# Optimization experiments

Measured on AMD Instinct MI355X. Metric: run time of the kernel, lower is better.

## Reference

```python
import jax, jax.numpy as jnp
import numpy as np


def setup_inputs() -> dict:
    key = jax.random.key(0)
    ks = jax.random.split(key, 7)
    B, N, D, A = 32, 128, 512, 512
    sD = 1.0 / np.sqrt(D)
    sA = 1.0 / np.sqrt(A)
    return {
        "x": jax.random.normal(ks[0], (B, N, D), dtype=jnp.float32),
        "W1": jax.random.normal(ks[1], (A, D), dtype=jnp.float32) * sD,
        "b1": jax.random.normal(ks[2], (A,), dtype=jnp.float32) * sD,
        "W2": jax.random.normal(ks[3], (A, D), dtype=jnp.float32) * sD,
        "b2": jax.random.normal(ks[4], (A,), dtype=jnp.float32) * sD,
        "Wout": jax.random.normal(ks[5], (A,), dtype=jnp.float32) * sA,
        "bout": jax.random.normal(ks[6], (1,), dtype=jnp.float32) * sA,
    }


def reference(x, W1, b1, W2, b2, Wout, bout):
    # x: (B, N, D)
    x1 = jnp.einsum('bnd,ad->bna', x, W1) + b1  # mlp1 -> (B, N, A)
    x2 = jnp.einsum('bnd,ad->bna', x, W2) + b2  # mlp2 -> (B, N, A)
    # outer broadcast add: x1.unsqueeze(1) + x2.unsqueeze(2) -> (B, N, N, A)
    s = x1[:, None, :, :] + x2[:, :, None, :]
    # include_root=False: drop ROOT row along dim 1 -> (B, N-1, N, A)
    s = s[:, 1:, :, :]
    s = jnp.tanh(s)
    # out linear A -> 1, then squeeze -> (B, N-1, N)
    return jnp.einsum('bija,a->bij', s, Wout) + bout[0]
```

## Files before the change

kernel.cpp:

```cpp
#include <hip/hip_runtime.h>
#include <hip/hip_bf16.h>

#define B_ 32
#define N_ 128
#define D_ 512
#define A_ 512
#define R_ (B_*N_)
#define OC 1024
#define CEXP 2.8853900817779268f

typedef __attribute__((ext_vector_type(8)))  short frag_ab;
typedef __attribute__((ext_vector_type(16))) float frag_c;

__device__ inline unsigned pack2bf(float a, float b) {
    unsigned ua = __builtin_bit_cast(unsigned, a) + 0x8000u;
    unsigned ub = __builtin_bit_cast(unsigned, b) + 0x8000u;
    return __builtin_amdgcn_perm(ub, ua, 0x07060302);
}
__device__ inline float bf2f_lo(unsigned u){ return __builtin_bit_cast(float, u << 16); }
__device__ inline float bf2f_hi(unsigned u){ return __builtin_bit_cast(float, u & 0xffff0000u); }

__global__ __launch_bounds__(256) void k0_cvt(
    const float* __restrict__ X, const float* __restrict__ W1,
    const float* __restrict__ W2,
    unsigned short* __restrict__ Xb, unsigned short* __restrict__ W1b,
    unsigned short* __restrict__ W2b)
{
    const int NX = R_*D_/8, NW = A_*D_/8;
    int i = blockIdx.x*256 + threadIdx.x;
    const float* src; unsigned short* dst; int off;
    if (i < NX)            { src = X;  dst = Xb;  off = i; }
    else if (i < NX+NW)    { src = W1; dst = W1b; off = i-NX; }
    else if (i < NX+2*NW)  { src = W2; dst = W2b; off = i-NX-NW; }
    else return;
    float4 a = ((const float4*)src)[off*2];
    float4 c = ((const float4*)src)[off*2+1];
    uint4 o;
    o.x = pack2bf(a.x,a.y); o.y = pack2bf(a.z,a.w);
    o.z = pack2bf(c.x,c.y); o.w = pack2bf(c.z,c.w);
    ((uint4*)dst)[off] = o;
}

__global__ __launch_bounds__(256) void k1_mfma(
    const unsigned short* __restrict__ Xb,
    const unsigned short* __restrict__ W1b, const float* __restrict__ b1,
    const unsigned short* __restrict__ W2b, const float* __restrict__ b2,
    unsigned short* __restrict__ Yb)
{
    __shared__ unsigned short As[2][64*64];
    __shared__ unsigned short Bs[2][64*64];

    const int t = threadIdx.x, lane = t&63, wid = t>>6;
    const int wr = wid>>1, wc = wid&1;
    const int row0 = blockIdx.x*64, col0 = blockIdx.y*64;
    const unsigned short* Wb = (col0 < A_) ? W1b : W2b;
    const float* bb = (col0 < A_) ? b1 : b2;
    const int wrow0 = col0 & (A_-1);

    const int sr = t>>2;
    const int ss = (t&3)*2;
    const int sf = sr & 7;

    frag_c acc;
#pragma unroll
    for (int r=0;r<16;++r) acc[r] = 0.f;

    const int fr = lane & 31;
    const int hs = lane >> 5;
    const int arow = wr*32 + fr, af_f = arow & 7;
    const int brow = wc*32 + fr, bf_f = brow & 7;

    {
        const unsigned short* px = &Xb[(size_t)(row0 +sr)*D_ + ss*8];
        const unsigned short* pw = &Wb[(size_t)(wrow0+sr)*D_ + ss*8];
        uint4 a0 = *(const uint4*)px, a1 = *(const uint4*)(px+8);
        uint4 b0 = *(const uint4*)pw, b1v = *(const uint4*)(pw+8);
        *(uint4*)&As[0][sr*64 + (( ss   ^sf)<<3)] = a0;
        *(uint4*)&As[0][sr*64 + (((ss+1)^sf)<<3)] = a1;
        *(uint4*)&Bs[0][sr*64 + (( ss   ^sf)<<3)] = b0;
        *(uint4*)&Bs[0][sr*64 + (((ss+1)^sf)<<3)] = b1v;
    }
    __syncthreads();

#pragma unroll
    for (int s = 0; s < 8; ++s) {
        const int cur = s & 1;
        uint4 a0, a1, b0, b1v;
        if (s < 7) {
            const int k0 = (s+1)*64;
            const unsigned short* px = &Xb[(size_t)(row0 +sr)*D_ + k0 + ss*8];
            const unsigned short* pw = &Wb[(size_t)(wrow0+sr)*D_ + k0 + ss*8];
            a0 = *(const uint4*)px; a1 = *(const uint4*)(px+8);
            b0 = *(const uint4*)pw; b1v = *(const uint4*)(pw+8);
        }
        frag_ab af[4], bf[4];
#pragma unroll
        for (int ks=0; ks<4; ++ks) {
            const int slot = ks*2 + hs;
            af[ks] = *(const frag_ab*)&As[cur][arow*64 + ((slot^af_f)<<3)];
            bf[ks] = *(const frag_ab*)&Bs[cur][brow*64 + ((slot^bf_f)<<3)];
        }
#pragma unroll
        for (int ks=0; ks<4; ++ks)
            acc = __builtin_amdgcn_mfma_f32_32x32x16_bf16(af[ks], bf[ks], acc, 0, 0, 0);
        if (s < 7) {
            *(uint4*)&As[cur^1][sr*64 + (( ss   ^sf)<<3)] = a0;
            *(uint4*)&As[cur^1][sr*64 + (((ss+1)^sf)<<3)] = a1;
            *(uint4*)&Bs[cur^1][sr*64 + (( ss   ^sf)<<3)] = b0;
            *(uint4*)&Bs[cur^1][sr*64 + (((ss+1)^sf)<<3)] = b1v;
        }
        __syncthreads();
    }

    const int cc = col0 + wc*32 + (lane&31);
    const float bias = bb[cc & (A_-1)];
    const int rbase = row0 + wr*32 + 4*(lane>>5);
#pragma unroll
    for (int r=0; r<16; ++r) {
        const int rr = rbase + (r&3) + 8*(r>>2);
        float e = __builtin_amdgcn_exp2f(CEXP*(acc[r] + bias));
        Yb[(size_t)rr*OC + cc] =
            (unsigned short)((__builtin_bit_cast(unsigned, e) + 0x8000u) >> 16);
    }
}

__global__ __launch_bounds__(256) void k2_tanh(
    const unsigned short* __restrict__ Yb,
    const float* __restrict__ Wout,
    float* __restrict__ P)
{
    __shared__ unsigned short e1s[64*64];
    __shared__ unsigned short e2s[64*64];
    __shared__ float wo[64];
    __shared__ float wsum_s;

    const int t  = threadIdx.x;
    const int jt = blockIdx.x & 1;
    const int it = blockIdx.x >> 1;
    const int ac = blockIdx.y;
    const int b  = blockIdx.z;
    const int abase = ac*64;

    if (t < 64) {
        float w = Wout[abase + t];
        wo[t] = w;
#pragma unroll
        for (int off=32; off>=1; off>>=1) w += __shfl_down(w, off, 64);
        if (t == 0) wsum_s = w;
    }

    const unsigned short* yb = Yb + (size_t)b*N_*OC;
    {
        const int r  = t>>2;
        const int s0 = (t&3)*2;
        const int f  = (r>>2)&7;
        int g2 = it*64 + r + 1; if (g2 > 127) g2 = 127;
        const unsigned short* p1 = &yb[(size_t)(jt*64 + r)*OC + abase + s0*8];
        const unsigned short* p2 = &yb[(size_t)g2*OC + A_ + abase + s0*8];
        uint4 a0 = *(const uint4*)p1, a1 = *(const uint4*)(p1+8);
        uint4 b0 = *(const uint4*)p2, b1v = *(const uint4*)(p2+8);
        *(uint4*)&e1s[r*64 + (( s0   ^f)<<3)] = a0;
        *(uint4*)&e1s[r*64 + (((s0+1)^f)<<3)] = a1;
        *(uint4*)&e2s[r*64 + (( s0   ^f)<<3)] = b0;
        *(uint4*)&e2s[r*64 + (((s0+1)^f)<<3)] = b1v;
    }
    __syncthreads();

    const int jl = t&15, il = t>>4;
    const int fj = jl&7, fi = il&7;
    float acc[4][4];
#pragma unroll
    for (int kj=0;kj<4;++kj)
#pragma unroll
        for (int ki=0;ki<4;++ki) acc[kj][ki] = 0.f;

#pragma unroll
    for (int c8=0; c8<8; ++c8) {
        uint4 V4[4];
#pragma unroll
        for (int ki=0;ki<4;++ki)
            V4[ki] = *(const uint4*)&e2s[(4*il+ki)*64 + ((c8^fi)<<3)];
        float vf[4][8];
#pragma unroll
        for (int ki=0;ki<4;++ki) {
            vf[ki][0]=bf2f_lo(V4[ki].x); vf[ki][1]=bf2f_hi(V4[ki].x);
            vf[ki][2]=bf2f_lo(V4[ki].y); vf[ki][3]=bf2f_hi(V4[ki].y);
            vf[ki][4]=bf2f_lo(V4[ki].z); vf[ki][5]=bf2f_hi(V4[ki].z);
            vf[ki][6]=bf2f_lo(V4[ki].w); vf[ki][7]=bf2f_hi(V4[ki].w);
        }
        float4 wa = *(const float4*)&wo[c8*8];
        float4 wb = *(const float4*)&wo[c8*8 + 4];
#pragma unroll
        for (int kj=0;kj<4;++kj) {
            uint4 U = *(const uint4*)&e1s[(4*jl+kj)*64 + ((c8^fj)<<3)];
            float u0=bf2f_lo(U.x), u1=bf2f_hi(U.x), u2=bf2f_lo(U.y), u3=bf2f_hi(U.y);
            float u4=bf2f_lo(U.z), u5=bf2f_hi(U.z), u6=bf2f_lo(U.w), u7=bf2f_hi(U.w);
#pragma unroll
            for (int ki=0;ki<4;++ki) {
                { float r0=fmaf(u0,vf[ki][0],1.f), s0=fmaf(u1,vf[ki][1],1.f);
                  acc[kj][ki]=fmaf(fmaf(wa.x,s0,wa.y*r0),__builtin_amdgcn_rcpf(r0*s0),acc[kj][ki]); }
                { float r0=fmaf(u2,vf[ki][2],1.f), s0=fmaf(u3,vf[ki][3],1.f);
                  acc[kj][ki]=fmaf(fmaf(wa.z,s0,wa.w*r0),__builtin_amdgcn_rcpf(r0*s0),acc[kj][ki]); }
                { float r0=fmaf(u4,vf[ki][4],1.f), s0=fmaf(u5,vf[ki][5],1.f);
                  acc[kj][ki]=fmaf(fmaf(wb.x,s0,wb.y*r0),__builtin_amdgcn_rcpf(r0*s0),acc[kj][ki]); }
                { float r0=fmaf(u6,vf[ki][6],1.f), s0=fmaf(u7,vf[ki][7],1.f);
                  acc[kj][ki]=fmaf(fmaf(wb.z,s0,wb.w*r0),__builtin_amdgcn_rcpf(r0*s0),acc[kj][ki]); }
            }
        }
    }

    const float base = wsum_s;
    float* Pb = P + ((size_t)(ac*B_ + b))*128*128;
#pragma unroll
    for (int ki=0;ki<4;++ki) {
        const int i0 = it*64 + 4*il + ki;
        float4 o = { base - 2.f*acc[0][ki], base - 2.f*acc[1][ki],
                     base - 2.f*acc[2][ki], base - 2.f*acc[3][ki] };
        *(float4*)&Pb[i0*128 + jt*64 + 4*jl] = o;
    }
}

__global__ __launch_bounds__(256) void k3_reduce(
    const float* __restrict__ P, const float* __restrict__ bout,
    float* __restrict__ out)
{
    int o = blockIdx.x*256 + threadIdx.x;
    if (o >= B_*127*128) return;
    const int b = o / (127*128);
    const int rem = o - b*127*128;
    const float* p = P + (size_t)b*16384 + rem;
    float s = bout[0];
#pragma unroll
    for (int q=0; q<8; ++q) s += p[(size_t)q*B_*16384];
    out[o] = s;
}

extern "C" void kernel_launch(void* const* d_in, const int* in_sizes, int n_in,
                              void* d_out, int out_size, void* d_ws, size_t ws_size,
                              hipStream_t stream) {
    const float* x    = (const float*)d_in[0];
    const float* W1   = (const float*)d_in[1];
    const float* b1   = (const float*)d_in[2];
    const float* W2   = (const float*)d_in[3];
    const float* b2   = (const float*)d_in[4];
    const float* Wout = (const float*)d_in[5];
    const float* bout = (const float*)d_in[6];
    float* out = (float*)d_out;

    char* ws = (char*)d_ws;
    unsigned short* Yb  = (unsigned short*)ws;
    unsigned short* Xb  = (unsigned short*)(ws + (8u<<20));
    unsigned short* W1b = (unsigned short*)(ws + (12u<<20));
    unsigned short* W2b = (unsigned short*)(ws + (12u<<20) + (1u<<19));
    float*          P   = (float*)(ws + (16u<<20));

    k0_cvt<<<1280, 256, 0, stream>>>(x, W1, W2, Xb, W1b, W2b);

    dim3 g1(R_/64, OC/64);
    k1_mfma<<<g1, 256, 0, stream>>>(Xb, W1b, b1, W2b, b2, Yb);

    dim3 g2(4, 8, B_);
    k2_tanh<<<g2, 256, 0, stream>>>(Yb, Wout, P);

    k3_reduce<<<(B_*127*128 + 255)/256, 256, 0, stream>>>(P, bout, out);
}
```

Baseline: 122.9 us.

## Fuse bf16 conversion into GEMM and full-A reduction into tanh kernel

The separate fp32-to-bf16 conversion kernel is dropped, and the GEMM now loads fp32 X/W and packs to bf16 while staging into LDS. The pairwise tanh kernel now handles the whole 512-wide A dimension per block, using 32x32 tiles with a 2x2 micro-tile per thread. It writes final outputs with bout directly, which removes the partial-sum buffer P and the k3 reduction launch. The cost is twice the global load bytes in the GEMM, lower ILP per thread in k2, and fewer blocks (512 versus 1024).

Result: slower. 125.9 us (+2.4%).

```diff
diff --git a/kernel.cpp b/kernel.cpp
--- a/kernel.cpp
+++ b/kernel.cpp
@@ -20,31 +20,10 @@
 __device__ inline float bf2f_lo(unsigned u){ return __builtin_bit_cast(float, u << 16); }
 __device__ inline float bf2f_hi(unsigned u){ return __builtin_bit_cast(float, u & 0xffff0000u); }
 
-__global__ __launch_bounds__(256) void k0_cvt(
-    const float* __restrict__ X, const float* __restrict__ W1,
-    const float* __restrict__ W2,
-    unsigned short* __restrict__ Xb, unsigned short* __restrict__ W1b,
-    unsigned short* __restrict__ W2b)
-{
-    const int NX = R_*D_/8, NW = A_*D_/8;
-    int i = blockIdx.x*256 + threadIdx.x;
-    const float* src; unsigned short* dst; int off;
-    if (i < NX)            { src = X;  dst = Xb;  off = i; }
-    else if (i < NX+NW)    { src = W1; dst = W1b; off = i-NX; }
-    else if (i < NX+2*NW)  { src = W2; dst = W2b; off = i-NX-NW; }
-    else return;
-    float4 a = ((const float4*)src)[off*2];
-    float4 c = ((const float4*)src)[off*2+1];
-    uint4 o;
-    o.x = pack2bf(a.x,a.y); o.y = pack2bf(a.z,a.w);
-    o.z = pack2bf(c.x,c.y); o.w = pack2bf(c.z,c.w);
-    ((uint4*)dst)[off] = o;
-}
-
 __global__ __launch_bounds__(256) void k1_mfma(
-    const unsigned short* __restrict__ Xb,
-    const unsigned short* __restrict__ W1b, const float* __restrict__ b1,
-    const unsigned short* __restrict__ W2b, const float* __restrict__ b2,
+    const float* __restrict__ X,
+    const float* __restrict__ W1, const float* __restrict__ b1,
+    const float* __restrict__ W2, const float* __restrict__ b2,
     unsigned short* __restrict__ Yb)
 {
     __shared__ unsigned short As[2][64*64];
@@ -53,7 +32,7 @@
     const int t = threadIdx.x, lane = t&63, wid = t>>6;
     const int wr = wid>>1, wc = wid&1;
     const int row0 = blockIdx.x*64, col0 = blockIdx.y*64;
-    const unsigned short* Wb = (col0 < A_) ? W1b : W2b;
+    const float* Wb = (col0 < A_) ? W1 : W2;
     const float* bb = (col0 < A_) ? b1 : b2;
     const int wrow0 = col0 & (A_-1);
 
@@ -70,28 +49,35 @@
     const int arow = wr*32 + fr, af_f = arow & 7;
     const int brow = wc*32 + fr, bf_f = brow & 7;
 
+    const float* pxb = &X [(size_t)(row0 +sr)*D_ + ss*8];
+    const float* pwb = &Wb[(size_t)(wrow0+sr)*D_ + ss*8];
+
     {
-        const unsigned short* px = &Xb[(size_t)(row0 +sr)*D_ + ss*8];
-        const unsigned short* pw = &Wb[(size_t)(wrow0+sr)*D_ + ss*8];
-        uint4 a0 = *(const uint4*)px, a1 = *(const uint4*)(px+8);
-        uint4 b0 = *(const uint4*)pw, b1v = *(const uint4*)(pw+8);
-        *(uint4*)&As[0][sr*64 + (( ss   ^sf)<<3)] = a0;
-        *(uint4*)&As[0][sr*64 + (((ss+1)^sf)<<3)] = a1;
-        *(uint4*)&Bs[0][sr*64 + (( ss   ^sf)<<3)] = b0;
-        *(uint4*)&Bs[0][sr*64 + (((ss+1)^sf)<<3)] = b1v;
+        float4 x0 = *(const float4*)pxb,     x1 = *(const float4*)(pxb+4);
+        float4 x2 = *(const float4*)(pxb+8), x3 = *(const float4*)(pxb+12);
+        float4 w0 = *(const float4*)pwb,     w1 = *(const float4*)(pwb+4);
+        float4 w2 = *(const float4*)(pwb+8), w3 = *(const float4*)(pwb+12);
+        uint4 A0 = {pack2bf(x0.x,x0.y), pack2bf(x0.z,x0.w), pack2bf(x1.x,x1.y), pack2bf(x1.z,x1.w)};
+        uint4 A1 = {pack2bf(x2.x,x2.y), pack2bf(x2.z,x2.w), pack2bf(x3.x,x3.y), pack2bf(x3.z,x3.w)};
+        uint4 B0 = {pack2bf(w0.x,w0.y), pack2bf(w0.z,w0.w), pack2bf(w1.x,w1.y), pack2bf(w1.z,w1.w)};
+        uint4 B1 = {pack2bf(w2.x,w2.y), pack2bf(w2.z,w2.w), pack2bf(w3.x,w3.y), pack2bf(w3.z,w3.w)};
+        *(uint4*)&As[0][sr*64 + (( ss   ^sf)<<3)] = A0;
+        *(uint4*)&As[0][sr*64 + (((ss+1)^sf)<<3)] = A1;
+        *(uint4*)&Bs[0][sr*64 + (( ss   ^sf)<<3)] = B0;
+        *(uint4*)&Bs[0][sr*64 + (((ss+1)^sf)<<3)] = B1;
     }
     __syncthreads();
 
 #pragma unroll
     for (int s = 0; s < 8; ++s) {
         const int cur = s & 1;
-        uint4 a0, a1, b0, b1v;
+        float4 x0,x1,x2,x3,w0,w1,w2,w3;
         if (s < 7) {
             const int k0 = (s+1)*64;
-            const unsigned short* px = &Xb[(size_t)(row0 +sr)*D_ + k0 + ss*8];
-            const unsigned short* pw = &Wb[(size_t)(wrow0+sr)*D_ + k0 + ss*8];
-            a0 = *(const uint4*)px; a1 = *(const uint4*)(px+8);
-            b0 = *(const uint4*)pw; b1v = *(const uint4*)(pw+8);
+            x0 = *(const float4*)(pxb+k0);    x1 = *(const float4*)(pxb+k0+4);
+            x2 = *(const float4*)(pxb+k0+8);  x3 = *(const float4*)(pxb+k0+12);
+            w0 = *(const float4*)(pwb+k0);    w1 = *(const float4*)(pwb+k0+4);
+            w2 = *(const float4*)(pwb+k0+8);  w3 = *(const float4*)(pwb+k0+12);
         }
         frag_ab af[4], bf[4];
 #pragma unroll
@@ -104,10 +90,14 @@
         for (int ks=0; ks<4; ++ks)
             acc = __builtin_amdgcn_mfma_f32_32x32x16_bf16(af[ks], bf[ks], acc, 0, 0, 0);
         if (s < 7) {
-            *(uint4*)&As[cur^1][sr*64 + (( ss   ^sf)<<3)] = a0;
-            *(uint4*)&As[cur^1][sr*64 + (((ss+1)^sf)<<3)] = a1;
-            *(uint4*)&Bs[cur^1][sr*64 + (( ss   ^sf)<<3)] = b0;
-            *(uint4*)&Bs[cur^1][sr*64 + (((ss+1)^sf)<<3)] = b1v;
+            uint4 A0 = {pack2bf(x0.x,x0.y), pack2bf(x0.z,x0.w), pack2bf(x1.x,x1.y), pack2bf(x1.z,x1.w)};
+            uint4 A1 = {pack2bf(x2.x,x2.y), pack2bf(x2.z,x2.w), pack2bf(x3.x,x3.y), pack2bf(x3.z,x3.w)};
+            uint4 B0 = {pack2bf(w0.x,w0.y), pack2bf(w0.z,w0.w), pack2bf(w1.x,w1.y), pack2bf(w1.z,w1.w)};
+            uint4 B1 = {pack2bf(w2.x,w2.y), pack2bf(w2.z,w2.w), pack2bf(w3.x,w3.y), pack2bf(w3.z,w3.w)};
+            *(uint4*)&As[cur^1][sr*64 + (( ss   ^sf)<<3)] = A0;
+            *(uint4*)&As[cur^1][sr*64 + (((ss+1)^sf)<<3)] = A1;
+            *(uint4*)&Bs[cur^1][sr*64 + (( ss   ^sf)<<3)] = B0;
+            *(uint4*)&Bs[cur^1][sr*64 + (((ss+1)^sf)<<3)] = B1;
         }
         __syncthreads();
     }
@@ -126,113 +116,95 @@
 
 __global__ __launch_bounds__(256) void k2_tanh(
     const unsigned short* __restrict__ Yb,
-    const float* __restrict__ Wout,
-    float* __restrict__ P)
+    const float* __restrict__ Wout, const float* __restrict__ bout,
+    float* __restrict__ out)
 {
-    __shared__ unsigned short e1s[64*64];
-    __shared__ unsigned short e2s[64*64];
-    __shared__ float wo[64];
-    __shared__ float wsum_s;
+    __shared__ unsigned short e1s[32*512];
+    __shared__ unsigned short e2s[32*512];
+    __shared__ float wo[A_];
+    __shared__ float wsum_s[4];
 
     const int t  = threadIdx.x;
-    const int jt = blockIdx.x & 1;
-    const int it = blockIdx.x >> 1;
-    const int ac = blockIdx.y;
-    const int b  = blockIdx.z;
-    const int abase = ac*64;
-
-    if (t < 64) {
-        float w = Wout[abase + t];
-        wo[t] = w;
-#pragma unroll
-        for (int off=32; off>=1; off>>=1) w += __shfl_down(w, off, 64);
-        if (t == 0) wsum_s = w;
+    const int jt = blockIdx.x & 3;
+    const int it = blockIdx.x >> 2;
+    const int b  = blockIdx.y;
+
+    {
+        float w0 = Wout[t], w1 = Wout[256+t];
+        wo[t] = w0; wo[256+t] = w1;
+        float s = w0 + w1;
+#pragma unroll
+        for (int off=32; off>=1; off>>=1) s += __shfl_down(s, off, 64);
+        if ((t&63)==0) wsum_s[t>>6] = s;
     }
 
     const unsigned short* yb = Yb + (size_t)b*N_*OC;
     {
-        const int r  = t>>2;
-        const int s0 = (t&3)*2;
-        const int f  = (r>>2)&7;
-        int g2 = it*64 + r + 1; if (g2 > 127) g2 = 127;
-        const unsigned short* p1 = &yb[(size_t)(jt*64 + r)*OC + abase + s0*8];
-        const unsigned short* p2 = &yb[(size_t)g2*OC + A_ + abase + s0*8];
-        uint4 a0 = *(const uint4*)p1, a1 = *(const uint4*)(p1+8);
-        uint4 b0 = *(const uint4*)p2, b1v = *(const uint4*)(p2+8);
-        *(uint4*)&e1s[r*64 + (( s0   ^f)<<3)] = a0;
-        *(uint4*)&e1s[r*64 + (((s0+1)^f)<<3)] = a1;
-        *(uint4*)&e2s[r*64 + (( s0   ^f)<<3)] = b0;
-        *(uint4*)&e2s[r*64 + (((s0+1)^f)<<3)] = b1v;
+        const int r = t>>3, inner = t&7;
+        const int key = r >> 1;
+        const int g2 = min(it*32 + r + 1, 127);
+        const unsigned short* p1 = &yb[(size_t)(jt*32 + r)*OC + inner*8];
+        const unsigned short* p2 = &yb[(size_t)g2*OC + A_ + inner*8];
+        unsigned short* d1 = &e1s[r*512];
+        unsigned short* d2 = &e2s[r*512];
+#pragma unroll
+        for (int q=0; q<8; ++q) {
+            const int slot = q*8 + inner;
+            uint4 v1 = *(const uint4*)(p1 + q*64);
+            uint4 v2 = *(const uint4*)(p2 + q*64);
+            *(uint4*)&d1[(slot^key)<<3] = v1;
+            *(uint4*)&d2[(slot^key)<<3] = v2;
+        }
     }
     __syncthreads();
 
     const int jl = t&15, il = t>>4;
-    const int fj = jl&7, fi = il&7;
-    float acc[4][4];
-#pragma unroll
-    for (int kj=0;kj<4;++kj)
-#pragma unroll
-        for (int ki=0;ki<4;++ki) acc[kj][ki] = 0.f;
-
-#pragma unroll
-    for (int c8=0; c8<8; ++c8) {
-        uint4 V4[4];
-#pragma unroll
-        for (int ki=0;ki<4;++ki)
-            V4[ki] = *(const uint4*)&e2s[(4*il+ki)*64 + ((c8^fi)<<3)];
-        float vf[4][8];
-#pragma unroll
-        for (int ki=0;ki<4;++ki) {
-            vf[ki][0]=bf2f_lo(V4[ki].x); vf[ki][1]=bf2f_hi(V4[ki].x);
-            vf[ki][2]=bf2f_lo(V4[ki].y); vf[ki][3]=bf2f_hi(V4[ki].y);
-            vf[ki][4]=bf2f_lo(V4[ki].z); vf[ki][5]=bf2f_hi(V4[ki].z);
-            vf[ki][6]=bf2f_lo(V4[ki].w); vf[ki][7]=bf2f_hi(V4[ki].w);
-        }
+    const unsigned short* ru0 = &e1s[(2*jl  )*512];
+    const unsigned short* ru1 = &e1s[(2*jl+1)*512];
+    const unsigned short* rv0 = &e2s[(2*il  )*512];
+    const unsigned short* rv1 = &e2s[(2*il+1)*512];
+
+    float a00=0.f, a01=0.f, a10=0.f, a11=0.f;
+
+#pragma unroll 2
+    for (int c8=0; c8<64; ++c8) {
+        uint4 U0 = *(const uint4*)&ru0[(c8^jl)<<3];
+        uint4 U1 = *(const uint4*)&ru1[(c8^jl)<<3];
+        uint4 V0 = *(const uint4*)&rv0[(c8^il)<<3];
+        uint4 V1 = *(const uint4*)&rv1[(c8^il)<<3];
         float4 wa = *(const float4*)&wo[c8*8];
-        float4 wb = *(const float4*)&wo[c8*8 + 4];
-#pragma unroll
-        for (int kj=0;kj<4;++kj) {
-            uint4 U = *(const uint4*)&e1s[(4*jl+kj)*64 + ((c8^fj)<<3)];
-            float u0=bf2f_lo(U.x), u1=bf2f_hi(U.x), u2=bf2f_lo(U.y), u3=bf2f_hi(U.y);
-            float u4=bf2f_lo(U.z), u5=bf2f_hi(U.z), u6=bf2f_lo(U.w), u7=bf2f_hi(U.w);
-#pragma unroll
-            for (int ki=0;ki<4;++ki) {
-                { float r0=fmaf(u0,vf[ki][0],1.f), s0=fmaf(u1,vf[ki][1],1.f);
-                  acc[kj][ki]=fmaf(fmaf(wa.x,s0,wa.y*r0),__builtin_amdgcn_rcpf(r0*s0),acc[kj][ki]); }
-                { float r0=fmaf(u2,vf[ki][2],1.f), s0=fmaf(u3,vf[ki][3],1.f);
-                  acc[kj][ki]=fmaf(fmaf(wa.z,s0,wa.w*r0),__builtin_amdgcn_rcpf(r0*s0),acc[kj][ki]); }
-                { float r0=fmaf(u4,vf[ki][4],1.f), s0=fmaf(u5,vf[ki][5],1.f);
-                  acc[kj][ki]=fmaf(fmaf(wb.x,s0,wb.y*r0),__builtin_amdgcn_rcpf(r0*s0),acc[kj][ki]); }
-                { float r0=fmaf(u6,vf[ki][6],1.f), s0=fmaf(u7,vf[ki][7],1.f);
-                  acc[kj][ki]=fmaf(fmaf(wb.z,s0,wb.w*r0),__builtin_amdgcn_rcpf(r0*s0),acc[kj][ki]); }
-            }
-        }
-    }
-
-    const float base = wsum_s;
-    float* Pb = P + ((size_t)(ac*B_ + b))*128*128;
-#pragma unroll
-    for (int ki=0;ki<4;++ki) {
-        const int i0 = it*64 + 4*il + ki;
-        float4 o = { base - 2.f*acc[0][ki], base - 2.f*acc[1][ki],
-                     base - 2.f*acc[2][ki], base - 2.f*acc[3][ki] };
-        *(float4*)&Pb[i0*128 + jt*64 + 4*jl] = o;
-    }
-}
-
-__global__ __launch_bounds__(256) void k3_reduce(
-    const float* __restrict__ P, const float* __restrict__ bout,
-    float* __restrict__ out)
-{
-    int o = blockIdx.x*256 + threadIdx.x;
-    if (o >= B_*127*128) return;
-    const int b = o / (127*128);
-    const int rem = o - b*127*128;
-    const float* p = P + (size_t)b*16384 + rem;
-    float s = bout[0];
-#pragma unroll
-    for (int q=0; q<8; ++q) s += p[(size_t)q*B_*16384];
-    out[o] = s;
+        float4 wb = *(const float4*)&wo[c8*8+4];
+        float u0[8], u1[8], v0[8], v1[8];
+        u0[0]=bf2f_lo(U0.x); u0[1]=bf2f_hi(U0.x); u0[2]=bf2f_lo(U0.y); u0[3]=bf2f_hi(U0.y);
+        u0[4]=bf2f_lo(U0.z); u0[5]=bf2f_hi(U0.z); u0[6]=bf2f_lo(U0.w); u0[7]=bf2f_hi(U0.w);
+        u1[0]=bf2f_lo(U1.x); u1[1]=bf2f_hi(U1.x); u1[2]=bf2f_lo(U1.y); u1[3]=bf2f_hi(U1.y);
+        u1[4]=bf2f_lo(U1.z); u1[5]=bf2f_hi(U1.z); u1[6]=bf2f_lo(U1.w); u1[7]=bf2f_hi(U1.w);
+        v0[0]=bf2f_lo(V0.x); v0[1]=bf2f_hi(V0.x); v0[2]=bf2f_lo(V0.y); v0[3]=bf2f_hi(V0.y);
+        v0[4]=bf2f_lo(V0.z); v0[5]=bf2f_hi(V0.z); v0[6]=bf2f_lo(V0.w); v0[7]=bf2f_hi(V0.w);
+        v1[0]=bf2f_lo(V1.x); v1[1]=bf2f_hi(V1.x); v1[2]=bf2f_lo(V1.y); v1[3]=bf2f_hi(V1.y);
+        v1[4]=bf2f_lo(V1.z); v1[5]=bf2f_hi(V1.z); v1[6]=bf2f_lo(V1.w); v1[7]=bf2f_hi(V1.w);
+        float wf[8] = {wa.x, wa.y, wa.z, wa.w, wb.x, wb.y, wb.z, wb.w};
+#pragma unroll
+        for (int p=0; p<4; ++p) {
+            const int e0 = 2*p, e1 = 2*p+1;
+            { float r=fmaf(u0[e0],v0[e0],1.f), s=fmaf(u0[e1],v0[e1],1.f);
+              a00 = fmaf(fmaf(wf[e0],s,wf[e1]*r), __builtin_amdgcn_rcpf(r*s), a00); }
+            { float r=fmaf(u1[e0],v0[e0],1.f), s=fmaf(u1[e1],v0[e1],1.f);
+              a10 = fmaf(fmaf(wf[e0],s,wf[e1]*r), __builtin_amdgcn_rcpf(r*s), a10); }
+            { float r=fmaf(u0[e0],v1[e0],1.f), s=fmaf(u0[e1],v1[e1],1.f);
+              a01 = fmaf(fmaf(wf[e0],s,wf[e1]*r), __builtin_amdgcn_rcpf(r*s), a01); }
+            { float r=fmaf(u1[e0],v1[e0],1.f), s=fmaf(u1[e1],v1[e1],1.f);
+              a11 = fmaf(fmaf(wf[e0],s,wf[e1]*r), __builtin_amdgcn_rcpf(r*s), a11); }
+        }
+    }
+
+    const float base = wsum_s[0]+wsum_s[1]+wsum_s[2]+wsum_s[3] + bout[0];
+    const int i0 = it*32 + 2*il;
+    const int j0 = jt*32 + 2*jl;
+    float* ob = out + (size_t)b*127*128;
+    *(float2*)&ob[i0*128 + j0] = float2{base - 2.f*a00, base - 2.f*a10};
+    if (i0 + 1 < 127)
+        *(float2*)&ob[(i0+1)*128 + j0] = float2{base - 2.f*a01, base - 2.f*a11};
 }
 
 extern "C" void kernel_launch(void* const* d_in, const int* in_sizes, int n_in,
@@ -247,20 +219,11 @@
     const float* bout = (const float*)d_in[6];
     float* out = (float*)d_out;
 
-    char* ws = (char*)d_ws;
-    unsigned short* Yb  = (unsigned short*)ws;
-    unsigned short* Xb  = (unsigned short*)(ws + (8u<<20));
-    unsigned short* W1b = (unsigned short*)(ws + (12u<<20));
-    unsigned short* W2b = (unsigned short*)(ws + (12u<<20) + (1u<<19));
-    float*          P   = (float*)(ws + (16u<<20));
-
-    k0_cvt<<<1280, 256, 0, stream>>>(x, W1, W2, Xb, W1b, W2b);
+    unsigned short* Yb = (unsigned short*)d_ws;
 
     dim3 g1(R_/64, OC/64);
-    k1_mfma<<<g1, 256, 0, stream>>>(Xb, W1b, b1, W2b, b2, Yb);
-
-    dim3 g2(4, 8, B_);
-    k2_tanh<<<g2, 256, 0, stream>>>(Yb, Wout, P);
-
-    k3_reduce<<<(B_*127*128 + 255)/256, 256, 0, stream>>>(P, bout, out);
-}
+    k1_mfma<<<g1, 256, 0, stream>>>(x, W1, b1, W2, b2, Yb);
+
+    dim3 g2(16, B_);
+    k2_tanh<<<g2, 256, 0, stream>>>(Yb, Wout, bout, out);
+}
```

## Fuse A-dimension reduction into tanh kernel and drop partial-sum buffer

Applied to the files above, without the earlier changes.

The tanh kernel now loops over the full A dimension in two 256-wide LDS chunks, so each block writes final outputs (with bout added) directly. This removes the per-chunk partial-sum buffer P, its global write and read, and the separate reduction kernel launch. To keep the grid size, each block covers a smaller 16x32 output tile and each thread computes two outputs instead of sixteen. That gives much less register reuse and more LDS reads per tanh evaluation.

Result: faster. 118.9 us (-3.3%).

```diff
diff --git a/kernel.cpp b/kernel.cpp
--- a/kernel.cpp
+++ b/kernel.cpp
@@ -124,115 +124,98 @@
     }
 }
 
+#define ACH2 256
+
 __global__ __launch_bounds__(256) void k2_tanh(
     const unsigned short* __restrict__ Yb,
-    const float* __restrict__ Wout,
-    float* __restrict__ P)
-{
-    __shared__ unsigned short e1s[64*64];
-    __shared__ unsigned short e2s[64*64];
-    __shared__ float wo[64];
-    __shared__ float wsum_s;
-
-    const int t  = threadIdx.x;
-    const int jt = blockIdx.x & 1;
-    const int it = blockIdx.x >> 1;
-    const int ac = blockIdx.y;
-    const int b  = blockIdx.z;
-    const int abase = ac*64;
-
-    if (t < 64) {
-        float w = Wout[abase + t];
-        wo[t] = w;
-#pragma unroll
-        for (int off=32; off>=1; off>>=1) w += __shfl_down(w, off, 64);
-        if (t == 0) wsum_s = w;
-    }
-
-    const unsigned short* yb = Yb + (size_t)b*N_*OC;
-    {
-        const int r  = t>>2;
-        const int s0 = (t&3)*2;
-        const int f  = (r>>2)&7;
-        int g2 = it*64 + r + 1; if (g2 > 127) g2 = 127;
-        const unsigned short* p1 = &yb[(size_t)(jt*64 + r)*OC + abase + s0*8];
-        const unsigned short* p2 = &yb[(size_t)g2*OC + A_ + abase + s0*8];
-        uint4 a0 = *(const uint4*)p1, a1 = *(const uint4*)(p1+8);
-        uint4 b0 = *(const uint4*)p2, b1v = *(const uint4*)(p2+8);
-        *(uint4*)&e1s[r*64 + (( s0   ^f)<<3)] = a0;
-        *(uint4*)&e1s[r*64 + (((s0+1)^f)<<3)] = a1;
-        *(uint4*)&e2s[r*64 + (( s0   ^f)<<3)] = b0;
-        *(uint4*)&e2s[r*64 + (((s0+1)^f)<<3)] = b1v;
-    }
-    __syncthreads();
-
-    const int jl = t&15, il = t>>4;
-    const int fj = jl&7, fi = il&7;
-    float acc[4][4];
-#pragma unroll
-    for (int kj=0;kj<4;++kj)
-#pragma unroll
-        for (int ki=0;ki<4;++ki) acc[kj][ki] = 0.f;
-
-#pragma unroll
-    for (int c8=0; c8<8; ++c8) {
-        uint4 V4[4];
-#pragma unroll
-        for (int ki=0;ki<4;++ki)
-            V4[ki] = *(const uint4*)&e2s[(4*il+ki)*64 + ((c8^fi)<<3)];
-        float vf[4][8];
-#pragma unroll
-        for (int ki=0;ki<4;++ki) {
-            vf[ki][0]=bf2f_lo(V4[ki].x); vf[ki][1]=bf2f_hi(V4[ki].x);
-            vf[ki][2]=bf2f_lo(V4[ki].y); vf[ki][3]=bf2f_hi(V4[ki].y);
-            vf[ki][4]=bf2f_lo(V4[ki].z); vf[ki][5]=bf2f_hi(V4[ki].z);
-            vf[ki][6]=bf2f_lo(V4[ki].w); vf[ki][7]=bf2f_hi(V4[ki].w);
-        }
-        float4 wa = *(const float4*)&wo[c8*8];
-        float4 wb = *(const float4*)&wo[c8*8 + 4];
-#pragma unroll
-        for (int kj=0;kj<4;++kj) {
-            uint4 U = *(const uint4*)&e1s[(4*jl+kj)*64 + ((c8^fj)<<3)];
-            float u0=bf2f_lo(U.x), u1=bf2f_hi(U.x), u2=bf2f_lo(U.y), u3=bf2f_hi(U.y);
-            float u4=bf2f_lo(U.z), u5=bf2f_hi(U.z), u6=bf2f_lo(U.w), u7=bf2f_hi(U.w);
-#pragma unroll
-            for (int ki=0;ki<4;++ki) {
-                { float r0=fmaf(u0,vf[ki][0],1.f), s0=fmaf(u1,vf[ki][1],1.f);
-                  acc[kj][ki]=fmaf(fmaf(wa.x,s0,wa.y*r0),__builtin_amdgcn_rcpf(r0*s0),acc[kj][ki]); }
-                { float r0=fmaf(u2,vf[ki][2],1.f), s0=fmaf(u3,vf[ki][3],1.f);
-                  acc[kj][ki]=fmaf(fmaf(wa.z,s0,wa.w*r0),__builtin_amdgcn_rcpf(r0*s0),acc[kj][ki]); }
-                { float r0=fmaf(u4,vf[ki][4],1.f), s0=fmaf(u5,vf[ki][5],1.f);
-                  acc[kj][ki]=fmaf(fmaf(wb.x,s0,wb.y*r0),__builtin_amdgcn_rcpf(r0*s0),acc[kj][ki]); }
-                { float r0=fmaf(u6,vf[ki][6],1.f), s0=fmaf(u7,vf[ki][7],1.f);
-                  acc[kj][ki]=fmaf(fmaf(wb.z,s0,wb.w*r0),__builtin_amdgcn_rcpf(r0*s0),acc[kj][ki]); }
-            }
-        }
-    }
-
-    const float base = wsum_s;
-    float* Pb = P + ((size_t)(ac*B_ + b))*128*128;
-#pragma unroll
-    for (int ki=0;ki<4;++ki) {
-        const int i0 = it*64 + 4*il + ki;
-        float4 o = { base - 2.f*acc[0][ki], base - 2.f*acc[1][ki],
-                     base - 2.f*acc[2][ki], base - 2.f*acc[3][ki] };
-        *(float4*)&Pb[i0*128 + jt*64 + 4*jl] = o;
-    }
-}
-
-__global__ __launch_bounds__(256) void k3_reduce(
-    const float* __restrict__ P, const float* __restrict__ bout,
+    const float* __restrict__ Wout, const float* __restrict__ bout,
     float* __restrict__ out)
 {
-    int o = blockIdx.x*256 + threadIdx.x;
-    if (o >= B_*127*128) return;
-    const int b = o / (127*128);
-    const int rem = o - b*127*128;
-    const float* p = P + (size_t)b*16384 + rem;
-    float s = bout[0];
-#pragma unroll
-    for (int q=0; q<8; ++q) s += p[(size_t)q*B_*16384];
-    out[o] = s;
+    __shared__ unsigned short e1s[32*ACH2];
+    __shared__ unsigned short e2s[16*ACH2];
+    __shared__ float wo[A_];
+    __shared__ float wsum_s[4];
+
+    const int t  = threadIdx.x;
+    const int jt = blockIdx.x;
+    const int it = blockIdx.y;
+    const int b  = blockIdx.z;
+
+    {
+        float w0 = Wout[t], w1 = Wout[256+t];
+        wo[t] = w0; wo[256+t] = w1;
+        float s = w0 + w1;
+#pragma unroll
+        for (int off=32; off>=1; off>>=1) s += __shfl_down(s, off, 64);
+        if ((t&63)==0) wsum_s[t>>6] = s;
+    }
+
+    const unsigned short* yb = Yb + (size_t)b*N_*OC;
+    const int jl = t&15, il = t>>4;
+
+    const int r1 = t>>3,  in1 = t&7;
+    const int r2 = t>>4,  in2 = t&15;
+    const int g2 = min(it*16 + r2 + 1, 127);
+    const unsigned short* p1 = &yb[(size_t)(jt*32 + r1)*OC];
+    const unsigned short* p2 = &yb[(size_t)g2*OC + A_];
+
+    float acc0 = 0.f, acc1 = 0.f;
+
+#pragma unroll
+    for (int ch = 0; ch < 2; ++ch) {
+        const int abase = ch*ACH2;
+        if (ch) __syncthreads();
+#pragma unroll
+        for (int q=0; q<4; ++q) {
+            const int s = q*8 + in1;
+            uint4 v = *(const uint4*)(p1 + abase + s*8);
+            *(uint4*)&e1s[r1*ACH2 + ((s ^ (r1>>1))<<3)] = v;
+        }
+#pragma unroll
+        for (int q=0; q<2; ++q) {
+            const int s = q*16 + in2;
+            uint4 v = *(const uint4*)(p2 + abase + s*8);
+            *(uint4*)&e2s[r2*ACH2 + ((s ^ (r2>>1))<<3)] = v;
+        }
+        __syncthreads();
+
+        const unsigned short* ru0 = &e1s[(2*jl  )*ACH2];
+        const unsigned short* ru1 = &e1s[(2*jl+1)*ACH2];
+        const unsigned short* rv  = &e2s[il*ACH2];
+        const int kv = il>>1;
+
+#pragma unroll 4
+        for (int c8=0; c8<32; ++c8) {
+            uint4 U0 = *(const uint4*)&ru0[(c8^jl)<<3];
+            uint4 U1 = *(const uint4*)&ru1[(c8^jl)<<3];
+            uint4 V  = *(const uint4*)&rv [(c8^kv)<<3];
+            float4 wa = *(const float4*)&wo[abase + c8*8];
+            float4 wb = *(const float4*)&wo[abase + c8*8 + 4];
+            float u0[8], u1[8], vv[8];
+            u0[0]=bf2f_lo(U0.x); u0[1]=bf2f_hi(U0.x); u0[2]=bf2f_lo(U0.y); u0[3]=bf2f_hi(U0.y);
+            u0[4]=bf2f_lo(U0.z); u0[5]=bf2f_hi(U0.z); u0[6]=bf2f_lo(U0.w); u0[7]=bf2f_hi(U0.w);
+            u1[0]=bf2f_lo(U1.x); u1[1]=bf2f_hi(U1.x); u1[2]=bf2f_lo(U1.y); u1[3]=bf2f_hi(U1.y);
+            u1[4]=bf2f_lo(U1.z); u1[5]=bf2f_hi(U1.z); u1[6]=bf2f_lo(U1.w); u1[7]=bf2f_hi(U1.w);
+            vv[0]=bf2f_lo(V.x);  vv[1]=bf2f_hi(V.x);  vv[2]=bf2f_lo(V.y);  vv[3]=bf2f_hi(V.y);
+            vv[4]=bf2f_lo(V.z);  vv[5]=bf2f_hi(V.z);  vv[6]=bf2f_lo(V.w);  vv[7]=bf2f_hi(V.w);
+            float wf[8] = {wa.x, wa.y, wa.z, wa.w, wb.x, wb.y, wb.z, wb.w};
+#pragma unroll
+            for (int p=0; p<4; ++p) {
+                const int e0 = 2*p, e1i = 2*p+1;
+                { float r=fmaf(u0[e0],vv[e0],1.f), s=fmaf(u0[e1i],vv[e1i],1.f);
+                  acc0 = fmaf(fmaf(wf[e0],s,wf[e1i]*r), __builtin_amdgcn_rcpf(r*s), acc0); }
+                { float r=fmaf(u1[e0],vv[e0],1.f), s=fmaf(u1[e1i],vv[e1i],1.f);
+                  acc1 = fmaf(fmaf(wf[e0],s,wf[e1i]*r), __builtin_amdgcn_rcpf(r*s), acc1); }
+            }
+        }
+    }
+
+    const float base = wsum_s[0]+wsum_s[1]+wsum_s[2]+wsum_s[3] + bout[0];
+    const int i0 = it*16 + il;
+    const int j0 = jt*32 + 2*jl;
+    if (i0 < 127)
+        *(float2*)&out[((size_t)(b*127) + i0)*128 + j0] =
+            float2{base - 2.f*acc0, base - 2.f*acc1};
 }
 
 extern "C" void kernel_launch(void* const* d_in, const int* in_sizes, int n_in,
@@ -252,7 +235,6 @@
     unsigned short* Xb  = (unsigned short*)(ws + (8u<<20));
     unsigned short* W1b = (unsigned short*)(ws + (12u<<20));
     unsigned short* W2b = (unsigned short*)(ws + (12u<<20) + (1u<<19));
-    float*          P   = (float*)(ws + (16u<<20));
 
     k0_cvt<<<1280, 256, 0, stream>>>(x, W1, W2, Xb, W1b, W2b);
 
@@ -260,7 +242,5 @@
     k1_mfma<<<g1, 256, 0, stream>>>(Xb, W1b, b1, W2b, b2, Yb);
 
     dim3 g2(4, 8, B_);
-    k2_tanh<<<g2, 256, 0, stream>>>(Yb, Wout, P);
-
-    k3_reduce<<<(B_*127*128 + 255)/256, 256, 0, stream>>>(P, bout, out);
-}
+    k2_tanh<<<g2, 256, 0, stream>>>(Yb, Wout, bout, out);
+}
```
